# Performance work log

Hardware: AMD Instinct MI355X
Metric: run time of the kernel (lower is better)

## Reference

```python
import jax, jax.numpy as jnp
import numpy as np

N = 200000   # points in scene batch
M = 32       # backbone feature width (cfg.m)
P = 64       # proposals after clustering
D = 16       # self.output_dim
NUM_PARAMS = (D + 3) * D + D + D + 1  # 337 = weight_nums + bias_nums


def _bn(x, g, b, eps=1e-5):
    # BatchNorm1d, training-mode batch stats over the point/instance axis
    mu = x.mean(axis=0)
    var = x.var(axis=0)
    return (x - mu) * jax.lax.rsqrt(var + eps) * g + b


def setup_inputs() -> dict:
    key = jax.random.key(0)
    ks = jax.random.split(key, 16)
    s = 0.1
    return {
        "feats": jax.random.normal(ks[0], (N, M), jnp.float32),
        "coords": jax.random.normal(ks[1], (N, 3), jnp.float32),
        "inst_feats": jax.random.normal(ks[2], (P, M), jnp.float32),
        "centers": jax.random.normal(ks[3], (P, 3), jnp.float32),
        "mask_w1": jax.random.normal(ks[4], (M, M), jnp.float32) * s,
        "mask_g1": jnp.ones((M,), jnp.float32), "mask_b1": jnp.zeros((M,), jnp.float32),
        "mask_w2": jax.random.normal(ks[5], (M, M), jnp.float32) * s,
        "mask_g2": jnp.ones((M,), jnp.float32), "mask_b2": jnp.zeros((M,), jnp.float32),
        "mask_w3": jax.random.normal(ks[6], (M, M), jnp.float32) * s,
        "mask_g3": jnp.ones((M,), jnp.float32), "mask_b3": jnp.zeros((M,), jnp.float32),
        "mask_w_out": jax.random.normal(ks[7], (M, D), jnp.float32) * s,
        "mask_b_out": jnp.zeros((D,), jnp.float32),
        # before_embedding_tower: conv1d 1x1 m->16 no-bias, BN, ReLU
        "emb_w": jax.random.normal(ks[8], (M, D), jnp.float32) * s,
        "emb_g": jnp.ones((D,), jnp.float32), "emb_b": jnp.zeros((D,), jnp.float32),
        # controller: conv1d 1x1 16->337 (std=0.01 init, zero bias)
        "ctrl_w": jax.random.normal(ks[9], (D, NUM_PARAMS), jnp.float32) * 0.01,
        "ctrl_b": jnp.zeros((NUM_PARAMS,), jnp.float32),
    }


def reference(feats, coords, inst_feats, centers,
              mask_w1, mask_g1, mask_b1,
              mask_w2, mask_g2, mask_b2,
              mask_w3, mask_g3, mask_b3,
              mask_w_out, mask_b_out,
              emb_w, emb_g, emb_b,
              ctrl_w, ctrl_b):
    # --- mask tower: per-point 1x1 convs ---
    x = feats
    for w, g, b in ((mask_w1, mask_g1, mask_b1),
                    (mask_w2, mask_g2, mask_b2),
                    (mask_w3, mask_g3, mask_b3)):
        x = jax.nn.relu(_bn(x @ w, g, b))
    mask_feats = x @ mask_w_out + mask_b_out                      # [N, D]

    # --- controller: generate dynamic filters per proposal ---
    e = jax.nn.relu(_bn(inst_feats @ emb_w, emb_g, emb_b))        # [P, D]
    params = e @ ctrl_w + ctrl_b                                  # [P, 337]
    w1 = params[:, :(D + 3) * D].reshape(P, D, D + 3)             # [P, out=16, in=19]
    w2 = params[:, (D + 3) * D:(D + 3) * D + D]                   # [P, 16] (out=1)
    b1 = params[:, (D + 4) * D:(D + 4) * D + D]                   # [P, 16]
    b2 = params[:, (D + 4) * D + D:]                              # [P, 1]

    # --- dynamic conv over all points; input = [rel_coords(3) | mask_feats(16)] ---
    rel = coords[None, :, :] - centers[:, None, :]                # [P, N, 3]
    h = (jnp.einsum('pnc,pdc->pnd', rel, w1[:, :, :3])
         + jnp.einsum('nc,pdc->pnd', mask_feats, w1[:, :, 3:])
         + b1[:, None, :])                                        # [P, N, 16]
    h = jax.nn.relu(h)
    logits = jnp.einsum('pnd,pd->pn', h, w2) + b2                 # [P, N]
    return logits
```

## Files before the change

### kernel.cpp

```cpp
#include <hip/hip_runtime.h>
#include <hip/hip_bf16.h>
#include <math.h>

#define N_PTS 200000
#define M 32
#define P_INST 64
#define D 16
#define NP 337

#define NBL ((N_PTS + 255) / 256)
#define HPB 128
#define NBH ((N_PTS + HPB - 1) / HPB)

#define WS_PARAMS 0
#define WS_STATS  21568
#define WS_W2     21760
#define WS_B2     22784
#define WS_APACK  22912
#define WS_Y      104832

typedef __attribute__((ext_vector_type(8))) short short8v;
typedef __attribute__((ext_vector_type(4))) float floatx4;
typedef __attribute__((ext_vector_type(16))) float floatx16;

static __device__ __forceinline__ unsigned short f2bf(float v) {
    __hip_bfloat16 h = __float2bfloat16(v);
    return *reinterpret_cast<unsigned short*>(&h);
}

__global__ __launch_bounds__(1024) void k_prep(
    const float* __restrict__ inst, const float* __restrict__ emb_w,
    const float* __restrict__ emb_g, const float* __restrict__ emb_b,
    const float* __restrict__ ctrl_w, const float* __restrict__ ctrl_b,
    const float* __restrict__ centers,
    float* __restrict__ params, float* __restrict__ apackf,
    float* __restrict__ w2p, float* __restrict__ b2p)
{
    __shared__ float sInst[P_INST * M];
    __shared__ float sCW[D * NP];
    __shared__ float sE[P_INST * D];
    __shared__ float sA[D], sC[D];
    int t = threadIdx.x;
    int lane = t & 63, wv = t >> 6;

    for (int i = t; i < P_INST * M; i += 1024) sInst[i] = inst[i];
    for (int i = t; i < D * NP; i += 1024) sCW[i] = ctrl_w[i];
    __syncthreads();

    {
        int p = t >> 4, d = t & (D - 1);
        float acc = 0.f;
        #pragma unroll
        for (int k = 0; k < M; k++) acc = fmaf(sInst[p * M + k], emb_w[k * D + d], acc);
        sE[t] = acc;
    }
    __syncthreads();

    if (t < D) {
        float s = 0.f, q = 0.f;
        for (int p = 0; p < P_INST; p++) { float v = sE[p * D + t]; s += v; q += v * v; }
        float mu = s * (1.f / P_INST);
        float var = q * (1.f / P_INST) - mu * mu;
        float a = emb_g[t] * rsqrtf(var + 1e-5f);
        sA[t] = a;
        sC[t] = emb_b[t] - mu * a;
    }
    __syncthreads();

    {
        int d = t & (D - 1);
        sE[t] = fmaxf(sE[t] * sA[d] + sC[d], 0.f);
    }
    __syncthreads();

    #pragma unroll
    for (int pp = 0; pp < 4; pp++) {
        int p = wv * 4 + pp;
        float e[D];
        #pragma unroll
        for (int d = 0; d < D; d++) e[d] = sE[p * D + d];
        for (int q = lane; q < NP; q += 64) {
            float acc = ctrl_b[q];
            #pragma unroll
            for (int d = 0; d < D; d++) acc = fmaf(e[d], sCW[d * NP + q], acc);
            params[p * NP + q] = acc;
        }
    }
    __threadfence_block();
    __syncthreads();

    {
        int row = lane & 31;
        int d = row & 15, psub = row >> 4;
        #pragma unroll
        for (int half = 0; half < 2; half++) {
            int pp = wv + half * 16;
            int p = pp * 2 + psub;
            const float* prm = params + p * NP;
            float bias = prm[320 + d] - (centers[p * 3 + 0] * prm[d * 19 + 0]
                                       + centers[p * 3 + 1] * prm[d * 19 + 1]
                                       + centers[p * 3 + 2] * prm[d * 19 + 2]);
            #pragma unroll
            for (int kc = 0; kc < 2; kc++) {
                int kbase = kc * 16 + (lane >> 5) * 8;
                unsigned int w[4];
                #pragma unroll
                for (int i = 0; i < 4; i++) {
                    unsigned short lo = 0, hi = 0;
                    #pragma unroll
                    for (int h = 0; h < 2; h++) {
                        int k = kbase + 2 * i + h;
                        float v;
                        if (k < 19) v = prm[d * 19 + k];
                        else if (k == 19) v = bias;
                        else v = 0.f;
                        if (h == 0) lo = f2bf(v); else hi = f2bf(v);
                    }
                    w[i] = (unsigned)lo | ((unsigned)hi << 16);
                }
                uint4* dst = (uint4*)((char*)apackf + (size_t)pp * 2048
                                      + kc * 1024 + lane * 16);
                *dst = make_uint4(w[0], w[1], w[2], w[3]);
            }
        }
    }

    {
        int row = lane & 15, dummy = row; (void)dummy;
        #pragma unroll
        for (int pi = 0; pi < 4; pi++) {
            int p = wv + pi * 16;
            const float* prm = params + p * NP;
            if (lane < 16) w2p[p * 16 + lane] = prm[304 + lane];
            if (lane == 0) b2p[p] = prm[336];
        }
    }
}

template <int L>
__global__ __launch_bounds__(256) void k_layer(
    const float* __restrict__ feats, const float* __restrict__ W,
    const float* __restrict__ stats, float* __restrict__ ybuf,
    float* __restrict__ partials)
{
    __shared__ float tr[256 * 33];
    __shared__ float red2[2][8][32];
    int t = threadIdx.x;
    int n = blockIdx.x * 256 + t;
    bool valid = n < N_PTS;
    int nc = valid ? n : N_PTS - 1;

    const float* src = ((L == 0) ? feats : ybuf) + (size_t)nc * M;
    float x[M];
    #pragma unroll
    for (int q = 0; q < M / 4; q++) {
        float4 v = ((const float4*)src)[q];
        x[4*q] = v.x; x[4*q+1] = v.y; x[4*q+2] = v.z; x[4*q+3] = v.w;
    }
    if (L > 0) {
        const float* st = stats + (L - 1) * 64;
        #pragma unroll
        for (int j = 0; j < M; j++) x[j] = fmaxf(fmaf(x[j], st[j], st[32 + j]), 0.f);
    }
    float y[M];
    #pragma unroll
    for (int j = 0; j < M; j++) y[j] = 0.f;
    #pragma unroll
    for (int i = 0; i < M; i++) {
        float xi = x[i];
        #pragma unroll
        for (int j = 0; j < M; j++) y[j] = fmaf(xi, W[i * M + j], y[j]);
    }
    if (valid) {
        float4* dst = (float4*)(ybuf + (size_t)n * M);
        #pragma unroll
        for (int q = 0; q < M / 4; q++)
            dst[q] = make_float4(y[4*q], y[4*q+1], y[4*q+2], y[4*q+3]);
    } else {
        #pragma unroll
        for (int j = 0; j < M; j++) y[j] = 0.f;
    }

    #pragma unroll
    for (int j = 0; j < M; j++) tr[t * 33 + j] = y[j];
    __syncthreads();
    int c = t & 31, s = t >> 5;
    float S = 0.f, Q = 0.f;
    #pragma unroll
    for (int r = 0; r < 32; r++) {
        float v = tr[(s * 32 + r) * 33 + c];
        S += v; Q += v * v;
    }
    red2[0][s][c] = S;
    red2[1][s][c] = Q;
    __syncthreads();
    if (t < 64) {
        int cc = t & 31, k = t >> 5;
        float a = 0.f;
        #pragma unroll
        for (int sl = 0; sl < 8; sl++) a += red2[k][sl][cc];
        partials[(size_t)blockIdx.x * 64 + k * 32 + cc] = a;
    }
}

__global__ __launch_bounds__(256) void k_reduce(
    const float* __restrict__ partials,
    const float* __restrict__ g, const float* __restrict__ b,
    float* __restrict__ stats_out)
{
    int c = blockIdx.x;
    int t = threadIdx.x;
    int part = t >> 7;
    int i0 = t & 127;
    float s = 0.f;
    for (int i = i0; i < NBL; i += 128)
        s += partials[(size_t)i * 64 + part * 32 + c];
    __shared__ float sh[256];
    sh[t] = s;
    __syncthreads();
    #pragma unroll
    for (int off = 64; off; off >>= 1) {
        if ((t & 127) < off) sh[t] += sh[t + off];
        __syncthreads();
    }
    if (t == 0) {
        float S = sh[0], Q = sh[128];
        float mu = S * (1.f / N_PTS);
        float var = Q * (1.f / N_PTS) - mu * mu;
        float a = g[c] * rsqrtf(var + 1e-5f);
        stats_out[c] = a;
        stats_out[32 + c] = b[c] - mu * a;
    }
}

__global__ __launch_bounds__(512)
__attribute__((amdgpu_waves_per_eu(2, 4)))
void k_head(
    const float* __restrict__ ybuf, const float* __restrict__ coords,
    const float* __restrict__ w_out, const float* __restrict__ b_out,
    const float* __restrict__ stats, const float* __restrict__ w2p,
    const float* __restrict__ b2p, const float* __restrict__ apackf,
    float* __restrict__ out)
{
    __shared__ unsigned int zlds[HPB * 20];
    __shared__ float w2lds[32 * 32];
    __shared__ float b2lds[64];
    int t = threadIdx.x;
    int nblk = blockIdx.x * HPB;

    if (t < HPB) {
        int nc = nblk + t;
        if (nc >= N_PTS) nc = N_PTS - 1;
        const float* yr = ybuf + (size_t)nc * M;
        float x[M];
        #pragma unroll
        for (int q = 0; q < M / 4; q++) {
            float4 v = ((const float4*)yr)[q];
            x[4*q] = v.x; x[4*q+1] = v.y; x[4*q+2] = v.z; x[4*q+3] = v.w;
        }
        const float* st = stats + 128;
        #pragma unroll
        for (int j = 0; j < M; j++) x[j] = fmaxf(fmaf(x[j], st[j], st[32 + j]), 0.f);

        float mf[D];
        #pragma unroll
        for (int d = 0; d < D; d++) mf[d] = b_out[d];
        #pragma unroll
        for (int i = 0; i < M; i++) {
            float xi = x[i];
            #pragma unroll
            for (int d = 0; d < D; d++) mf[d] = fmaf(xi, w_out[i * D + d], mf[d]);
        }
        float z[20];
        z[0] = coords[(size_t)nc * 3 + 0];
        z[1] = coords[(size_t)nc * 3 + 1];
        z[2] = coords[(size_t)nc * 3 + 2];
        #pragma unroll
        for (int d = 0; d < D; d++) z[3 + d] = mf[d];
        z[19] = 1.0f;

        unsigned int zw[16];
        #pragma unroll
        for (int i = 0; i < 10; i++)
            zw[i] = (unsigned)f2bf(z[2 * i]) | ((unsigned)f2bf(z[2 * i + 1]) << 16);
        #pragma unroll
        for (int i = 10; i < 16; i++) zw[i] = 0u;
        uint4* zd = (uint4*)&zlds[t * 20];
        #pragma unroll
        for (int i = 0; i < 4; i++)
            zd[i] = make_uint4(zw[4*i], zw[4*i+1], zw[4*i+2], zw[4*i+3]);
    } else if (t < 256) {
        int t2 = t - 128;
        if (t2 < 64) b2lds[t2] = b2p[t2];
        #pragma unroll
        for (int e = 0; e < 8; e++) {
            int idx = t2 * 8 + e;
            int pp = idx >> 5;
            int rem = idx & 31;
            int hi = rem >> 4, reg = rem & 15;
            int R = (reg & 3) + 8 * (reg >> 2) + 4 * hi;
            int p = pp * 2 + (R >> 4), d = R & 15;
            w2lds[idx] = w2p[p * 16 + d];
        }
    }
    __syncthreads();

    int lane = t & 63, wv = t >> 6;
    int slab = wv & 3, ph = wv >> 2;
    int col = lane & 31, hi = lane >> 5;
    int n0 = nblk + slab * 32;
    int nn = n0 + col;
    bool wr = nn < N_PTS;

    const unsigned int* zrow = &zlds[(slab * 32 + col) * 20];
    short8v B1 = *(const short8v*)(zrow + hi * 4);
    short8v B2 = *(const short8v*)(zrow + 8 + hi * 4);

    const char* abase = (const char*)apackf + (size_t)(ph * 16) * 2048 + lane * 16;

    #pragma unroll 4
    for (int i = 0; i < 16; i++) {
        int pp = ph * 16 + i;
        short8v A1 = *(const short8v*)(abase + (size_t)i * 2048);
        short8v A2 = *(const short8v*)(abase + (size_t)i * 2048 + 1024);
        const float* w2r = &w2lds[pp * 32 + hi * 16];
        floatx4 w2a = *(const floatx4*)(w2r + 0);
        floatx4 w2b = *(const floatx4*)(w2r + 4);
        floatx4 w2c = *(const floatx4*)(w2r + 8);
        floatx4 w2d = *(const floatx4*)(w2r + 12);
        float b2 = b2lds[pp * 2 + hi];

        floatx16 acc = {};
        acc = __builtin_amdgcn_mfma_f32_32x32x16_bf16(A1, B1, acc, 0, 0, 0);
        acc = __builtin_amdgcn_mfma_f32_32x32x16_bf16(A2, B2, acc, 0, 0, 0);

        float pA = fmaxf(acc[0], 0.f) * w2a[0];
        pA = fmaf(fmaxf(acc[1], 0.f), w2a[1], pA);
        pA = fmaf(fmaxf(acc[2], 0.f), w2a[2], pA);
        pA = fmaf(fmaxf(acc[3], 0.f), w2a[3], pA);
        pA = fmaf(fmaxf(acc[4], 0.f), w2b[0], pA);
        pA = fmaf(fmaxf(acc[5], 0.f), w2b[1], pA);
        pA = fmaf(fmaxf(acc[6], 0.f), w2b[2], pA);
        pA = fmaf(fmaxf(acc[7], 0.f), w2b[3], pA);
        float pB = fmaxf(acc[8], 0.f) * w2c[0];
        pB = fmaf(fmaxf(acc[9], 0.f), w2c[1], pB);
        pB = fmaf(fmaxf(acc[10], 0.f), w2c[2], pB);
        pB = fmaf(fmaxf(acc[11], 0.f), w2c[3], pB);
        pB = fmaf(fmaxf(acc[12], 0.f), w2d[0], pB);
        pB = fmaf(fmaxf(acc[13], 0.f), w2d[1], pB);
        pB = fmaf(fmaxf(acc[14], 0.f), w2d[2], pB);
        pB = fmaf(fmaxf(acc[15], 0.f), w2d[3], pB);

        pA += __shfl_xor(pA, 32, 64);
        pB += __shfl_xor(pB, 32, 64);

        float vout = (hi ? pB : pA) + b2;
        if (wr) out[(size_t)(pp * 2 + hi) * N_PTS + nn] = vout;
    }
}

extern "C" void kernel_launch(void* const* d_in, const int* in_sizes, int n_in,
                              void* d_out, int out_size, void* d_ws, size_t ws_size,
                              hipStream_t stream) {
    const float* feats   = (const float*)d_in[0];
    const float* coords  = (const float*)d_in[1];
    const float* inst    = (const float*)d_in[2];
    const float* centers = (const float*)d_in[3];
    const float* mw1 = (const float*)d_in[4];
    const float* mg1 = (const float*)d_in[5];
    const float* mb1 = (const float*)d_in[6];
    const float* mw2 = (const float*)d_in[7];
    const float* mg2 = (const float*)d_in[8];
    const float* mb2 = (const float*)d_in[9];
    const float* mw3 = (const float*)d_in[10];
    const float* mg3 = (const float*)d_in[11];
    const float* mb3 = (const float*)d_in[12];
    const float* wout = (const float*)d_in[13];
    const float* bout = (const float*)d_in[14];
    const float* embw = (const float*)d_in[15];
    const float* embg = (const float*)d_in[16];
    const float* embb = (const float*)d_in[17];
    const float* cw   = (const float*)d_in[18];
    const float* cb   = (const float*)d_in[19];

    float* wsf      = (float*)d_ws;
    float* params   = wsf + WS_PARAMS;
    float* stats    = wsf + WS_STATS;
    float* w2p      = wsf + WS_W2;
    float* b2p      = wsf + WS_B2;
    float* apackf   = wsf + WS_APACK;
    float* ybuf     = wsf + WS_Y;
    float* out      = (float*)d_out;
    float* partials = (float*)d_out;

    k_prep<<<1, 1024, 0, stream>>>(inst, embw, embg, embb, cw, cb, centers,
                                   params, apackf, w2p, b2p);

    k_layer<0><<<NBL, 256, 0, stream>>>(feats, mw1, stats, ybuf, partials);
    k_reduce<<<32, 256, 0, stream>>>(partials, mg1, mb1, stats + 0);

    k_layer<1><<<NBL, 256, 0, stream>>>(feats, mw2, stats, ybuf, partials);
    k_reduce<<<32, 256, 0, stream>>>(partials, mg2, mb2, stats + 64);

    k_layer<2><<<NBL, 256, 0, stream>>>(feats, mw3, stats, ybuf, partials);
    k_reduce<<<32, 256, 0, stream>>>(partials, mg3, mb3, stats + 128);

    k_head<<<NBH, 512, 0, stream>>>(ybuf, coords, wout, bout, stats,
                                    w2p, b2p, apackf, out);
}
```

Before: 147.2 us.

## Reassign waves to proposal pairs across all slabs and prefetch A fragments

Each wave now handles 4 proposal pairs across all four 32-point slabs instead of 16 pairs on one slab. The B fragments for all slabs stay in registers, and the next pair's A fragments are prefetched from global memory while the current pair is computed. The aim is to cut the number of global A-fragment loads per wave and to hide their latency. In exchange each wave holds more registers, and the output stores now cover all 128 point columns of the block instead of one slab.

```diff
diff --git a/kernel.cpp b/kernel.cpp
--- a/kernel.cpp
+++ b/kernel.cpp
@@ -126,7 +126,6 @@
     }
 
     {
-        int row = lane & 15, dummy = row; (void)dummy;
         #pragma unroll
         for (int pi = 0; pi < 4; pi++) {
             int p = wv + pi * 16;
@@ -306,23 +305,29 @@
     __syncthreads();
 
     int lane = t & 63, wv = t >> 6;
-    int slab = wv & 3, ph = wv >> 2;
     int col = lane & 31, hi = lane >> 5;
-    int n0 = nblk + slab * 32;
-    int nn = n0 + col;
-    bool wr = nn < N_PTS;
-
-    const unsigned int* zrow = &zlds[(slab * 32 + col) * 20];
-    short8v B1 = *(const short8v*)(zrow + hi * 4);
-    short8v B2 = *(const short8v*)(zrow + 8 + hi * 4);
-
-    const char* abase = (const char*)apackf + (size_t)(ph * 16) * 2048 + lane * 16;
-
-    #pragma unroll 4
-    for (int i = 0; i < 16; i++) {
-        int pp = ph * 16 + i;
-        short8v A1 = *(const short8v*)(abase + (size_t)i * 2048);
-        short8v A2 = *(const short8v*)(abase + (size_t)i * 2048 + 1024);
+
+    short8v B1[4], B2[4];
+    #pragma unroll
+    for (int s = 0; s < 4; s++) {
+        const unsigned int* zrow = &zlds[(s * 32 + col) * 20];
+        B1[s] = *(const short8v*)(zrow + hi * 4);
+        B2[s] = *(const short8v*)(zrow + 8 + hi * 4);
+    }
+
+    const char* abase = (const char*)apackf + (size_t)(wv * 4) * 2048 + lane * 16;
+
+    short8v A1n = *(const short8v*)(abase);
+    short8v A2n = *(const short8v*)(abase + 1024);
+
+    #pragma unroll
+    for (int i = 0; i < 4; i++) {
+        int pp = wv * 4 + i;
+        short8v A1 = A1n, A2 = A2n;
+        if (i < 3) {
+            A1n = *(const short8v*)(abase + (size_t)(i + 1) * 2048);
+            A2n = *(const short8v*)(abase + (size_t)(i + 1) * 2048 + 1024);
+        }
         const float* w2r = &w2lds[pp * 32 + hi * 16];
         floatx4 w2a = *(const floatx4*)(w2r + 0);
         floatx4 w2b = *(const floatx4*)(w2r + 4);
@@ -330,32 +335,36 @@
         floatx4 w2d = *(const floatx4*)(w2r + 12);
         float b2 = b2lds[pp * 2 + hi];
 
-        floatx16 acc = {};
-        acc = __builtin_amdgcn_mfma_f32_32x32x16_bf16(A1, B1, acc, 0, 0, 0);
-        acc = __builtin_amdgcn_mfma_f32_32x32x16_bf16(A2, B2, acc, 0, 0, 0);
-
-        float pA = fmaxf(acc[0], 0.f) * w2a[0];
-        pA = fmaf(fmaxf(acc[1], 0.f), w2a[1], pA);
-        pA = fmaf(fmaxf(acc[2], 0.f), w2a[2], pA);
-        pA = fmaf(fmaxf(acc[3], 0.f), w2a[3], pA);
-        pA = fmaf(fmaxf(acc[4], 0.f), w2b[0], pA);
-        pA = fmaf(fmaxf(acc[5], 0.f), w2b[1], pA);
-        pA = fmaf(fmaxf(acc[6], 0.f), w2b[2], pA);
-        pA = fmaf(fmaxf(acc[7], 0.f), w2b[3], pA);
-        float pB = fmaxf(acc[8], 0.f) * w2c[0];
-        pB = fmaf(fmaxf(acc[9], 0.f), w2c[1], pB);
-        pB = fmaf(fmaxf(acc[10], 0.f), w2c[2], pB);
-        pB = fmaf(fmaxf(acc[11], 0.f), w2c[3], pB);
-        pB = fmaf(fmaxf(acc[12], 0.f), w2d[0], pB);
-        pB = fmaf(fmaxf(acc[13], 0.f), w2d[1], pB);
-        pB = fmaf(fmaxf(acc[14], 0.f), w2d[2], pB);
-        pB = fmaf(fmaxf(acc[15], 0.f), w2d[3], pB);
-
-        pA += __shfl_xor(pA, 32, 64);
-        pB += __shfl_xor(pB, 32, 64);
-
-        float vout = (hi ? pB : pA) + b2;
-        if (wr) out[(size_t)(pp * 2 + hi) * N_PTS + nn] = vout;
+        #pragma unroll
+        for (int s = 0; s < 4; s++) {
+            floatx16 acc = {};
+            acc = __builtin_amdgcn_mfma_f32_32x32x16_bf16(A1, B1[s], acc, 0, 0, 0);
+            acc = __builtin_amdgcn_mfma_f32_32x32x16_bf16(A2, B2[s], acc, 0, 0, 0);
+
+            float pA = fmaxf(acc[0], 0.f) * w2a[0];
+            pA = fmaf(fmaxf(acc[1], 0.f), w2a[1], pA);
+            pA = fmaf(fmaxf(acc[2], 0.f), w2a[2], pA);
+            pA = fmaf(fmaxf(acc[3], 0.f), w2a[3], pA);
+            pA = fmaf(fmaxf(acc[4], 0.f), w2b[0], pA);
+            pA = fmaf(fmaxf(acc[5], 0.f), w2b[1], pA);
+            pA = fmaf(fmaxf(acc[6], 0.f), w2b[2], pA);
+            pA = fmaf(fmaxf(acc[7], 0.f), w2b[3], pA);
+            float pB = fmaxf(acc[8], 0.f) * w2c[0];
+            pB = fmaf(fmaxf(acc[9], 0.f), w2c[1], pB);
+            pB = fmaf(fmaxf(acc[10], 0.f), w2c[2], pB);
+            pB = fmaf(fmaxf(acc[11], 0.f), w2c[3], pB);
+            pB = fmaf(fmaxf(acc[12], 0.f), w2d[0], pB);
+            pB = fmaf(fmaxf(acc[13], 0.f), w2d[1], pB);
+            pB = fmaf(fmaxf(acc[14], 0.f), w2d[2], pB);
+            pB = fmaf(fmaxf(acc[15], 0.f), w2d[3], pB);
+
+            pA += __shfl_xor(pA, 32, 64);
+            pB += __shfl_xor(pB, 32, 64);
+
+            int nn = nblk + s * 32 + col;
+            float vout = (hi ? pB : pA) + b2;
+            if (nn < N_PTS) out[(size_t)(pp * 2 + hi) * N_PTS + nn] = vout;
+        }
     }
 }
 
```

New measurement: 142.4 us. -3.3%, faster.
